# Performance work log

Hardware: AMD Instinct MI355X
Metric: run time of the kernel (lower is better)

## Reference

```python
import jax, jax.numpy as jnp
import numpy as np

B, S, E, H = 4, 2048, 1024, 16
D = E // H
EPS = 1e-6


def setup_inputs() -> dict:
    key = jax.random.key(0)
    ks = jax.random.split(key, 6)
    glorot = lambda k: jax.random.uniform(k, (E, E), jnp.float32,
                                          -np.sqrt(6.0 / (E + E)), np.sqrt(6.0 / (E + E)))
    return {
        "x": jax.random.normal(ks[0], (B, S, E), jnp.float32),
        "mask": jnp.zeros((B, 1, 1, S), jnp.float32),
        "Wq": glorot(ks[1]), "bq": jnp.zeros((E,), jnp.float32),
        "Wk": glorot(ks[2]), "bk": jnp.zeros((E,), jnp.float32),
        "Wv": glorot(ks[3]), "bv": jnp.zeros((E,), jnp.float32),
        "Wo": glorot(ks[4]), "bo": jnp.zeros((E,), jnp.float32),
        "gamma": jnp.ones((E,), jnp.float32),
        "beta": jnp.zeros((E,), jnp.float32),
    }


def _split_heads(t):
    # [B, S, E] -> [B, H, S, D]
    return t.reshape(B, S, H, D).transpose(0, 2, 1, 3)


def reference(x, mask, Wq, bq, Wk, bk, Wv, bv, Wo, bo, gamma, beta):
    q = _split_heads(x @ Wq + bq)
    k = _split_heads(x @ Wk + bk)
    v = _split_heads(x @ Wv + bv)
    # NOTE: original divides by sqrt(embedding_size), not sqrt(depth)
    scores = jnp.einsum("bhqd,bhkd->bhqk", q, k) / jnp.sqrt(jnp.float32(E))
    scores = scores + mask * (-1e9)
    attn = jax.nn.softmax(scores, axis=-1)
    ctx = jnp.einsum("bhqk,bhkd->bhqd", attn, v)
    ctx = ctx.transpose(0, 2, 1, 3).reshape(B, S, E)
    main_out = ctx @ Wo + bo
    # dropout is identity (is_training=False); residual is the raw input
    added = main_out + x
    mu = jnp.mean(added, axis=-1, keepdims=True)
    var = jnp.mean(jnp.square(added - mu), axis=-1, keepdims=True)
    return gamma * (added - mu) / jnp.sqrt(var + EPS) + beta
```

## Files before the change

### kernel.cpp

```cpp
#include <hip/hip_runtime.h>
#include <hip/hip_bf16.h>


typedef __bf16 bf16_t;
typedef __bf16 bf16x8 __attribute__((ext_vector_type(8)));
typedef __bf16 bf16x4v __attribute__((ext_vector_type(4)));
typedef float f32x4 __attribute__((ext_vector_type(4)));

#define LDS_AS __attribute__((address_space(3)))
#define GLB_AS __attribute__((address_space(1)))

__device__ __forceinline__ void async16(bf16_t* lds, const bf16_t* g) {
  __builtin_amdgcn_global_load_lds((GLB_AS void*)const_cast<bf16_t*>(g),
                                   (LDS_AS void*)lds, 16, 0, 0);
}

__device__ __forceinline__ f32x4 mfma16(bf16x8 a, bf16x8 b, f32x4 c) {
  return __builtin_amdgcn_mfma_f32_16x16x32_bf16(a, b, c, 0, 0, 0);
}

__device__ __forceinline__ float fast_exp2(float x) {
#if __has_builtin(__builtin_amdgcn_exp2f)
  return __builtin_amdgcn_exp2f(x);
#else
  return __expf(x * 0.6931471805599453f);
#endif
}

__global__ __launch_bounds__(256) void cvt_x(const float* __restrict__ x,
                                             bf16_t* __restrict__ xb)
{
  const size_t i = ((size_t)blockIdx.x * 256 + threadIdx.x) * 4;
  const float4 v = *(const float4*)(x + i);
  bf16x4v o;
  o[0] = (bf16_t)v.x; o[1] = (bf16_t)v.y; o[2] = (bf16_t)v.z; o[3] = (bf16_t)v.w;
  *(bf16x4v*)(xb + i) = o;
}

__global__ __launch_bounds__(256) void maskp_k(const float* __restrict__ m,
                                               float* __restrict__ ms)
{
  const int i = blockIdx.x * 256 + threadIdx.x;
  ms[i] = m[i] * (-1.442695e9f);
}

__global__ __launch_bounds__(256) void transpose_k(
    const float* __restrict__ w0, const float* __restrict__ w1,
    const float* __restrict__ w2, const float* __restrict__ w3,
    bf16_t* __restrict__ dst)
{
  __shared__ bf16_t tile[32][33];
  const float* src = (blockIdx.z == 0) ? w0 : (blockIdx.z == 1) ? w1
                   : (blockIdx.z == 2) ? w2 : w3;
  bf16_t* d = dst + (size_t)blockIdx.z * 1024 * 1024;
  const int bx = blockIdx.x * 32, by = blockIdx.y * 32;
  const int tx = threadIdx.x, ty = threadIdx.y;
#pragma unroll
  for (int r = 0; r < 32; r += 8)
    tile[ty + r][tx] = (bf16_t)src[(size_t)(by + ty + r) * 1024 + bx + tx];
  __syncthreads();
#pragma unroll
  for (int r = 0; r < 32; r += 8)
    d[(size_t)(bx + ty + r) * 1024 + by + tx] = tile[tx][ty + r];
}

__global__ __launch_bounds__(256) void gemm_qkv(
    const bf16_t* __restrict__ X, const bf16_t* __restrict__ WtAll,
    const float* __restrict__ bq, const float* __restrict__ bk,
    const float* __restrict__ bv,
    bf16_t* __restrict__ Qb, bf16_t* __restrict__ Kb, bf16_t* __restrict__ Vtb)
{
  __shared__ __align__(16) bf16_t As[128 * 64];
  __shared__ __align__(16) bf16_t Bs[128 * 64];

  const int z = blockIdx.z;
  const bf16_t* Bt = WtAll + (size_t)z * 1024 * 1024;
  const float* bias = (z == 0) ? bq : (z == 1) ? bk : bv;
  const int bm0 = blockIdx.x * 128;
  const int bn0 = blockIdx.y * 128;
  const int t = threadIdx.x;
  const int w = t >> 6, lane = t & 63;
  const int wm = w >> 1, wn = w & 1;
  const int l15 = lane & 15, quad = lane >> 4;
  const int srow8 = lane >> 3;
  const int sp8   = lane & 7;

  f32x4 acc[4][4] = {};

  for (int k0 = 0; k0 < 1024; k0 += 64) {
    __syncthreads();
#pragma unroll
    for (int i = 0; i < 4; ++i) {
      const int row = (w * 4 + i) * 8 + srow8;
      const int c = sp8 ^ (row & 7);
      async16(&As[row * 64 + sp8 * 8], X  + (size_t)(bm0 + row) * 1024 + k0 + c * 8);
      async16(&Bs[row * 64 + sp8 * 8], Bt + (size_t)(bn0 + row) * 1024 + k0 + c * 8);
    }
    __syncthreads();

    bf16x8 af[4][2], bfr[4][2];
#pragma unroll
    for (int mi = 0; mi < 4; ++mi) {
      const int r = wm * 64 + mi * 16 + l15;
#pragma unroll
      for (int kc = 0; kc < 2; ++kc) {
        const int pg = (kc * 4 + quad) ^ (r & 7);
        af[mi][kc] = *(const bf16x8*)&As[r * 64 + pg * 8];
      }
    }
#pragma unroll
    for (int ni = 0; ni < 4; ++ni) {
      const int r = wn * 64 + ni * 16 + l15;
#pragma unroll
      for (int kc = 0; kc < 2; ++kc) {
        const int pg = (kc * 4 + quad) ^ (r & 7);
        bfr[ni][kc] = *(const bf16x8*)&Bs[r * 64 + pg * 8];
      }
    }
#pragma unroll
    for (int kc = 0; kc < 2; ++kc)
#pragma unroll
      for (int mi = 0; mi < 4; ++mi)
#pragma unroll
        for (int ni = 0; ni < 4; ++ni)
          acc[mi][ni] = mfma16(af[mi][kc], bfr[ni][kc], acc[mi][ni]);
  }

  const float QSCALE = 0.045084220f;

#pragma unroll
  for (int ni = 0; ni < 4; ++ni) {
    const int n = bn0 + wn * 64 + ni * 16 + l15;
    const float bb = bias[n];
    const int h = n >> 6, dd = n & 63;
    if (z == 2) {
#pragma unroll
      for (int mi = 0; mi < 4; ++mi) {
        const int m0 = bm0 + wm * 64 + mi * 16 + quad * 4;
        const int bi = m0 >> 11, s = m0 & 2047;
        bf16x4v vk;
#pragma unroll
        for (int r = 0; r < 4; ++r) vk[r] = (bf16_t)(acc[mi][ni][r] + bb);
        *(bf16x4v*)&Vtb[((size_t)(bi * 16 + h) * 64 + dd) * 2048 + s] = vk;
      }
    } else {
#pragma unroll
      for (int mi = 0; mi < 4; ++mi) {
#pragma unroll
        for (int r = 0; r < 4; ++r) {
          const int m = bm0 + wm * 64 + mi * 16 + quad * 4 + r;
          const float v = acc[mi][ni][r] + bb;
          const int bi = m >> 11, s = m & 2047;
          if (z == 0)
            Qb[((size_t)(bi * 16 + h) * 2048 + s) * 64 + dd] = (bf16_t)(v * QSCALE);
          else
            Kb[((size_t)(bi * 16 + h) * 2048 + s) * 64 + dd] = (bf16_t)v;
        }
      }
    }
  }
}

__global__ __launch_bounds__(256) void attn_k(
    const bf16_t* __restrict__ Qb, const bf16_t* __restrict__ Kb,
    const bf16_t* __restrict__ Vtb, const float* __restrict__ maskS,
    bf16_t* __restrict__ Ctx)
{
  __shared__ __align__(16) bf16_t Ks[64 * 64];
  __shared__ __align__(16) bf16_t Vs[64 * 64];
  __shared__ __align__(16) bf16_t Ps[128 * 64];

  const int qt = blockIdx.x, bh = blockIdx.y;
  const int bi = bh >> 4, h = bh & 15;
  const int q0 = qt * 128;
  const bf16_t* Qh = Qb + (size_t)bh * 2048 * 64;
  const bf16_t* Kh = Kb + (size_t)bh * 2048 * 64;
  const bf16_t* Vh = Vtb + (size_t)bh * 64 * 2048;
  const float* mrow = maskS + bi * 2048;

  const int t = threadIdx.x;
  const int w = t >> 6, lane = t & 63;
  const int l15 = lane & 15, quad = lane >> 4;

  bf16x8 qb[2][2];
#pragma unroll
  for (int ni = 0; ni < 2; ++ni)
#pragma unroll
    for (int kc = 0; kc < 2; ++kc)
      qb[ni][kc] = *(const bf16x8*)&Qh[(size_t)(q0 + w * 32 + ni * 16 + l15) * 64
                                       + kc * 32 + quad * 8];

  bf16x8 ones;
#pragma unroll
  for (int i = 0; i < 8; ++i) ones[i] = (bf16_t)1.0f;

  f32x4 oacc[4][2] = {};
  f32x4 lacc[2] = {};

  const int srow = lane >> 3;
  const int sp = lane & 7;

  for (int j = 0; j < 32; ++j) {
    const int k0 = j * 64;
    __syncthreads();
#pragma unroll
    for (int i = 0; i < 2; ++i) {
      const int row = (w * 2 + i) * 8 + srow;
      const int c = sp ^ (row & 7);
      async16(&Ks[row * 64 + sp * 8], Kh + (size_t)(k0 + row) * 64 + c * 8);
      async16(&Vs[row * 64 + sp * 8], Vh + (size_t)row * 2048 + k0 + c * 8);
    }
    __syncthreads();

    f32x4 sacc[4][2];
#pragma unroll
    for (int mi = 0; mi < 4; ++mi) {
      const float4 mk = *(const float4*)&mrow[k0 + mi * 16 + quad * 4];
      f32x4 cinit; cinit[0] = mk.x; cinit[1] = mk.y; cinit[2] = mk.z; cinit[3] = mk.w;
#pragma unroll
      for (int ni = 0; ni < 2; ++ni) sacc[mi][ni] = cinit;
    }
    bf16x8 kf[4][2];
#pragma unroll
    for (int mi = 0; mi < 4; ++mi)
#pragma unroll
      for (int kc = 0; kc < 2; ++kc) {
        const int r = mi * 16 + l15;
        const int pg = (kc * 4 + quad) ^ (r & 7);
        kf[mi][kc] = *(const bf16x8*)&Ks[r * 64 + pg * 8];
      }
#pragma unroll
    for (int mi = 0; mi < 4; ++mi)
#pragma unroll
      for (int ni = 0; ni < 2; ++ni)
#pragma unroll
        for (int kc = 0; kc < 2; ++kc)
          sacc[mi][ni] = mfma16(kf[mi][kc], qb[ni][kc], sacc[mi][ni]);

#pragma unroll
    for (int ni = 0; ni < 2; ++ni) {
      const int row = w * 32 + ni * 16 + l15;
#pragma unroll
      for (int mi = 0; mi < 4; ++mi) {
        bf16x4v pk;
        pk[0] = (bf16_t)fast_exp2(sacc[mi][ni][0]);
        pk[1] = (bf16_t)fast_exp2(sacc[mi][ni][1]);
        pk[2] = (bf16_t)fast_exp2(sacc[mi][ni][2]);
        pk[3] = (bf16_t)fast_exp2(sacc[mi][ni][3]);
        const int pg = (mi * 2 + (quad >> 1)) ^ (row & 7);
        *(bf16x4v*)&Ps[row * 64 + pg * 8 + (quad & 1) * 4] = pk;
      }
    }

    bf16x8 av[4][2], pb[2][2];
#pragma unroll
    for (int ni = 0; ni < 2; ++ni)
#pragma unroll
      for (int kc = 0; kc < 2; ++kc) {
        const int row = w * 32 + ni * 16 + l15;
        const int pg = (kc * 4 + quad) ^ (row & 7);
        pb[ni][kc] = *(const bf16x8*)&Ps[row * 64 + pg * 8];
      }
#pragma unroll
    for (int mi = 0; mi < 4; ++mi)
#pragma unroll
      for (int kc = 0; kc < 2; ++kc) {
        const int r = mi * 16 + l15;
        const int pg = (kc * 4 + quad) ^ (r & 7);
        av[mi][kc] = *(const bf16x8*)&Vs[r * 64 + pg * 8];
      }
#pragma unroll
    for (int mi = 0; mi < 4; ++mi)
#pragma unroll
      for (int ni = 0; ni < 2; ++ni)
#pragma unroll
        for (int kc = 0; kc < 2; ++kc)
          oacc[mi][ni] = mfma16(av[mi][kc], pb[ni][kc], oacc[mi][ni]);
#pragma unroll
    for (int ni = 0; ni < 2; ++ni)
#pragma unroll
      for (int kc = 0; kc < 2; ++kc)
        lacc[ni] = mfma16(ones, pb[ni][kc], lacc[ni]);
  }

#pragma unroll
  for (int ni = 0; ni < 2; ++ni) {
    const float inv = 1.0f / lacc[ni][0];
    const int s = q0 + w * 32 + ni * 16 + l15;
#pragma unroll
    for (int mi = 0; mi < 4; ++mi) {
      bf16x4v o4;
      o4[0] = (bf16_t)(oacc[mi][ni][0] * inv);
      o4[1] = (bf16_t)(oacc[mi][ni][1] * inv);
      o4[2] = (bf16_t)(oacc[mi][ni][2] * inv);
      o4[3] = (bf16_t)(oacc[mi][ni][3] * inv);
      *(bf16x4v*)&Ctx[((size_t)bi * 2048 + s) * 1024 + h * 64 + mi * 16 + quad * 4] = o4;
    }
  }
}

__global__ __launch_bounds__(256) void gemm_proj(
    const bf16_t* __restrict__ Ctx, const bf16_t* __restrict__ WoT,
    const float* __restrict__ bo, const float* __restrict__ Xres,
    float* __restrict__ Add)
{
  __shared__ __align__(16) bf16_t As[128 * 64];
  __shared__ __align__(16) bf16_t Bs[128 * 64];

  const int bm0 = blockIdx.x * 128;
  const int bn0 = blockIdx.y * 128;
  const int t = threadIdx.x;
  const int w = t >> 6, lane = t & 63;
  const int wm = w >> 1, wn = w & 1;
  const int l15 = lane & 15, quad = lane >> 4;
  const int srow8 = lane >> 3;
  const int sp8   = lane & 7;

  f32x4 acc[4][4] = {};

  for (int k0 = 0; k0 < 1024; k0 += 64) {
    __syncthreads();
#pragma unroll
    for (int i = 0; i < 4; ++i) {
      const int row = (w * 4 + i) * 8 + srow8;
      const int c = sp8 ^ (row & 7);
      async16(&As[row * 64 + sp8 * 8], Ctx + (size_t)(bm0 + row) * 1024 + k0 + c * 8);
      async16(&Bs[row * 64 + sp8 * 8], WoT + (size_t)(bn0 + row) * 1024 + k0 + c * 8);
    }
    __syncthreads();

    bf16x8 af[4][2], bfr[4][2];
#pragma unroll
    for (int mi = 0; mi < 4; ++mi) {
      const int r = wm * 64 + mi * 16 + l15;
#pragma unroll
      for (int kc = 0; kc < 2; ++kc) {
        const int pg = (kc * 4 + quad) ^ (r & 7);
        af[mi][kc] = *(const bf16x8*)&As[r * 64 + pg * 8];
      }
    }
#pragma unroll
    for (int ni = 0; ni < 4; ++ni) {
      const int r = wn * 64 + ni * 16 + l15;
#pragma unroll
      for (int kc = 0; kc < 2; ++kc) {
        const int pg = (kc * 4 + quad) ^ (r & 7);
        bfr[ni][kc] = *(const bf16x8*)&Bs[r * 64 + pg * 8];
      }
    }
#pragma unroll
    for (int kc = 0; kc < 2; ++kc)
#pragma unroll
      for (int mi = 0; mi < 4; ++mi)
#pragma unroll
        for (int ni = 0; ni < 4; ++ni)
          acc[mi][ni] = mfma16(af[mi][kc], bfr[ni][kc], acc[mi][ni]);
  }

#pragma unroll
  for (int ni = 0; ni < 4; ++ni) {
    const int n = bn0 + wn * 64 + ni * 16 + l15;
    const float bb = bo[n];
#pragma unroll
    for (int mi = 0; mi < 4; ++mi) {
#pragma unroll
      for (int r = 0; r < 4; ++r) {
        const int m = bm0 + wm * 64 + mi * 16 + quad * 4 + r;
        Add[(size_t)m * 1024 + n] =
            acc[mi][ni][r] + bb + Xres[(size_t)m * 1024 + n];
      }
    }
  }
}

__global__ __launch_bounds__(256) void ln_k(
    const float* __restrict__ A, const float* __restrict__ gamma,
    const float* __restrict__ beta, float* __restrict__ out)
{
  __shared__ float red[8];
  const int row = blockIdx.x, t = threadIdx.x;
  const float4 v = ((const float4*)(A + (size_t)row * 1024))[t];
  float s = v.x + v.y + v.z + v.w;
#pragma unroll
  for (int o = 32; o >= 1; o >>= 1) s += __shfl_xor(s, o);
  if ((t & 63) == 0) red[t >> 6] = s;
  __syncthreads();
  const float mu = (red[0] + red[1] + red[2] + red[3]) * (1.0f / 1024.0f);
  const float dx = v.x - mu, dy = v.y - mu, dz = v.z - mu, dw = v.w - mu;
  float q = dx * dx + dy * dy + dz * dz + dw * dw;
#pragma unroll
  for (int o = 32; o >= 1; o >>= 1) q += __shfl_xor(q, o);
  if ((t & 63) == 0) red[4 + (t >> 6)] = q;
  __syncthreads();
  const float var = (red[4] + red[5] + red[6] + red[7]) * (1.0f / 1024.0f);
  const float rs = rsqrtf(var + 1e-6f);

  const int c0 = t * 4;
  float4 o4;
  o4.x = gamma[c0 + 0] * dx * rs + beta[c0 + 0];
  o4.y = gamma[c0 + 1] * dy * rs + beta[c0 + 1];
  o4.z = gamma[c0 + 2] * dz * rs + beta[c0 + 2];
  o4.w = gamma[c0 + 3] * dw * rs + beta[c0 + 3];
  *(float4*)(out + (size_t)row * 1024 + c0) = o4;
}

extern "C" void kernel_launch(void* const* d_in, const int* in_sizes, int n_in,
                              void* d_out, int out_size, void* d_ws, size_t ws_size,
                              hipStream_t stream)
{
  const float* x     = (const float*)d_in[0];
  const float* mask  = (const float*)d_in[1];
  const float* Wq    = (const float*)d_in[2];
  const float* bq    = (const float*)d_in[3];
  const float* Wk    = (const float*)d_in[4];
  const float* bk    = (const float*)d_in[5];
  const float* Wv    = (const float*)d_in[6];
  const float* bv    = (const float*)d_in[7];
  const float* Wo    = (const float*)d_in[8];
  const float* bo    = (const float*)d_in[9];
  const float* gamma = (const float*)d_in[10];
  const float* beta  = (const float*)d_in[11];
  float* out = (float*)d_out;

  bf16_t* Wt    = (bf16_t*)d_ws;
  bf16_t* Xb    = Wt + (size_t)4 * 1024 * 1024;
  bf16_t* Qb    = Xb + (size_t)8192 * 1024;
  bf16_t* Kb    = Qb + (size_t)8192 * 1024;
  bf16_t* Vtb   = Kb + (size_t)8192 * 1024;
  bf16_t* Ctx   = Vtb + (size_t)8192 * 1024;
  float*  Add   = (float*)(Ctx + (size_t)8192 * 1024);
  float*  maskS = Add + (size_t)8192 * 1024;

  cvt_x<<<8192, 256, 0, stream>>>(x, Xb);
  maskp_k<<<32, 256, 0, stream>>>(mask, maskS);
  transpose_k<<<dim3(32, 32, 4), dim3(32, 8), 0, stream>>>(Wq, Wk, Wv, Wo, Wt);
  gemm_qkv<<<dim3(64, 8, 3), 256, 0, stream>>>(Xb, Wt, bq, bk, bv, Qb, Kb, Vtb);
  attn_k<<<dim3(16, 64), 256, 0, stream>>>(Qb, Kb, Vtb, maskS, Ctx);
  gemm_proj<<<dim3(64, 8), 256, 0, stream>>>(Ctx, Wt + (size_t)3 * 1024 * 1024, bo, x, Add);
  ln_k<<<8192, 256, 0, stream>>>(Add, gamma, beta, out);
}
```

Before: 338.6 us.

## Load K/V fragments directly from global in attention and fuse mask prep into cvt

The attention kernel no longer stages K and V tiles through LDS with async loads and two barriers per iteration. Each wave now reads its K and V MFMA fragments straight from global memory, relying on L1/L2 for reuse across the four waves. The mask scaling kernel is also folded into the x conversion kernel as extra blocks, saving one launch. The trade is that every wave issues redundant global loads with no explicit prefetch, so latency may be exposed.

```diff
diff --git a/kernel.cpp b/kernel.cpp
--- a/kernel.cpp
+++ b/kernel.cpp
@@ -28,20 +28,24 @@
 }
 
 __global__ __launch_bounds__(256) void cvt_x(const float* __restrict__ x,
-                                             bf16_t* __restrict__ xb)
-{
-  const size_t i = ((size_t)blockIdx.x * 256 + threadIdx.x) * 4;
-  const float4 v = *(const float4*)(x + i);
-  bf16x4v o;
-  o[0] = (bf16_t)v.x; o[1] = (bf16_t)v.y; o[2] = (bf16_t)v.z; o[3] = (bf16_t)v.w;
-  *(bf16x4v*)(xb + i) = o;
-}
-
-__global__ __launch_bounds__(256) void maskp_k(const float* __restrict__ m,
-                                               float* __restrict__ ms)
-{
-  const int i = blockIdx.x * 256 + threadIdx.x;
-  ms[i] = m[i] * (-1.442695e9f);
+                                             bf16_t* __restrict__ xb,
+                                             const float* __restrict__ mask,
+                                             float* __restrict__ maskS)
+{
+  if (blockIdx.x < 8192) {
+    const size_t i = ((size_t)blockIdx.x * 256 + threadIdx.x) * 4;
+    const float4 v = *(const float4*)(x + i);
+    bf16x4v o;
+    o[0] = (bf16_t)v.x; o[1] = (bf16_t)v.y; o[2] = (bf16_t)v.z; o[3] = (bf16_t)v.w;
+    *(bf16x4v*)(xb + i) = o;
+  } else {
+    const size_t i = ((size_t)(blockIdx.x - 8192) * 256 + threadIdx.x) * 4;
+    const float4 v = *(const float4*)(mask + i);
+    float4 o;
+    o.x = v.x * (-1.442695e9f); o.y = v.y * (-1.442695e9f);
+    o.z = v.z * (-1.442695e9f); o.w = v.w * (-1.442695e9f);
+    *(float4*)(maskS + i) = o;
+  }
 }
 
 __global__ __launch_bounds__(256) void transpose_k(
@@ -166,8 +170,6 @@
     const bf16_t* __restrict__ Vtb, const float* __restrict__ maskS,
     bf16_t* __restrict__ Ctx)
 {
-  __shared__ __align__(16) bf16_t Ks[64 * 64];
-  __shared__ __align__(16) bf16_t Vs[64 * 64];
   __shared__ __align__(16) bf16_t Ps[128 * 64];
 
   const int qt = blockIdx.x, bh = blockIdx.y;
@@ -197,20 +199,22 @@
   f32x4 oacc[4][2] = {};
   f32x4 lacc[2] = {};
 
-  const int srow = lane >> 3;
-  const int sp = lane & 7;
-
   for (int j = 0; j < 32; ++j) {
     const int k0 = j * 64;
-    __syncthreads();
-#pragma unroll
-    for (int i = 0; i < 2; ++i) {
-      const int row = (w * 2 + i) * 8 + srow;
-      const int c = sp ^ (row & 7);
-      async16(&Ks[row * 64 + sp * 8], Kh + (size_t)(k0 + row) * 64 + c * 8);
-      async16(&Vs[row * 64 + sp * 8], Vh + (size_t)row * 2048 + k0 + c * 8);
-    }
-    __syncthreads();
+
+    bf16x8 kf[4][2], av[4][2];
+#pragma unroll
+    for (int mi = 0; mi < 4; ++mi)
+#pragma unroll
+      for (int kc = 0; kc < 2; ++kc)
+        kf[mi][kc] = *(const bf16x8*)&Kh[(size_t)(k0 + mi * 16 + l15) * 64
+                                         + kc * 32 + quad * 8];
+#pragma unroll
+    for (int mi = 0; mi < 4; ++mi)
+#pragma unroll
+      for (int kc = 0; kc < 2; ++kc)
+        av[mi][kc] = *(const bf16x8*)&Vh[(size_t)(mi * 16 + l15) * 2048
+                                         + k0 + kc * 32 + quad * 8];
 
     f32x4 sacc[4][2];
 #pragma unroll
@@ -220,15 +224,6 @@
 #pragma unroll
       for (int ni = 0; ni < 2; ++ni) sacc[mi][ni] = cinit;
     }
-    bf16x8 kf[4][2];
-#pragma unroll
-    for (int mi = 0; mi < 4; ++mi)
-#pragma unroll
-      for (int kc = 0; kc < 2; ++kc) {
-        const int r = mi * 16 + l15;
-        const int pg = (kc * 4 + quad) ^ (r & 7);
-        kf[mi][kc] = *(const bf16x8*)&Ks[r * 64 + pg * 8];
-      }
 #pragma unroll
     for (int mi = 0; mi < 4; ++mi)
 #pragma unroll
@@ -252,7 +247,7 @@
       }
     }
 
-    bf16x8 av[4][2], pb[2][2];
+    bf16x8 pb[2][2];
 #pragma unroll
     for (int ni = 0; ni < 2; ++ni)
 #pragma unroll
@@ -260,14 +255,6 @@
         const int row = w * 32 + ni * 16 + l15;
         const int pg = (kc * 4 + quad) ^ (row & 7);
         pb[ni][kc] = *(const bf16x8*)&Ps[row * 64 + pg * 8];
-      }
-#pragma unroll
-    for (int mi = 0; mi < 4; ++mi)
-#pragma unroll
-      for (int kc = 0; kc < 2; ++kc) {
-        const int r = mi * 16 + l15;
-        const int pg = (kc * 4 + quad) ^ (r & 7);
-        av[mi][kc] = *(const bf16x8*)&Vs[r * 64 + pg * 8];
       }
 #pragma unroll
     for (int mi = 0; mi < 4; ++mi)
@@ -431,8 +418,7 @@
   float*  Add   = (float*)(Ctx + (size_t)8192 * 1024);
   float*  maskS = Add + (size_t)8192 * 1024;
 
-  cvt_x<<<8192, 256, 0, stream>>>(x, Xb);
-  maskp_k<<<32, 256, 0, stream>>>(mask, maskS);
+  cvt_x<<<8200, 256, 0, stream>>>(x, Xb, mask, maskS);
   transpose_k<<<dim3(32, 32, 4), dim3(32, 8), 0, stream>>>(Wq, Wk, Wv, Wo, Wt);
   gemm_qkv<<<dim3(64, 8, 3), 256, 0, stream>>>(Xb, Wt, bq, bk, bv, Qb, Kb, Vtb);
   attn_k<<<dim3(16, 64), 256, 0, stream>>>(Qb, Kb, Vtb, maskS, Ctx);
```

After: 460.6 us. 1.36x slower.
